# Kernel tuning notes

Measured on AMD Instinct MI355X. Metric: run time of the kernel, lower is better.

The kernel has to match this reference:

```python
import jax, jax.numpy as jnp
import numpy as np

DIM = 768
HEADS = 12
EPS = 1e-5


def setup_inputs() -> dict:
    key = jax.random.key(0)
    ks = jax.random.split(key, 12)
    B, N, C = 2, 2048, DIM
    s = 1.0 / np.sqrt(C)
    return {
        "query": jax.random.normal(ks[0], (B, N, C), jnp.float32),
        "key_in": jax.random.normal(ks[1], (B, N, C), jnp.float32),
        "value": jax.random.normal(ks[2], (B, N, C), jnp.float32),
        "Wq": jax.random.normal(ks[3], (C, C), jnp.float32) * s,
        "bq": jnp.zeros((C,), jnp.float32),
        "Wk": jax.random.normal(ks[4], (C, C), jnp.float32) * s,
        "bk": jnp.zeros((C,), jnp.float32),
        "Wv": jax.random.normal(ks[5], (C, C), jnp.float32) * s,
        "bv": jnp.zeros((C,), jnp.float32),
        "Wo": jax.random.normal(ks[6], (C, C), jnp.float32) * s,
        "bo": jnp.zeros((C,), jnp.float32),
        "gamma": jnp.ones((C,), jnp.float32),
        "beta": jnp.zeros((C,), jnp.float32),
    }


def reference(query, key_in, value, Wq, bq, Wk, bk, Wv, bv, Wo, bo, gamma, beta):
    B, N, C = query.shape
    H = HEADS
    Dh = C // H
    scale = Dh ** (-0.5)
    # projections -> [B, H, N, Dh]
    q = (query @ Wq + bq).reshape(B, N, H, Dh).transpose(0, 2, 1, 3)
    k = (key_in @ Wk + bk).reshape(B, N, H, Dh).transpose(0, 2, 1, 3)
    v = (value @ Wv + bv).reshape(B, N, H, Dh).transpose(0, 2, 1, 3)
    attn = jnp.einsum("bhnd,bhmd->bhnm", q, k) * scale
    attn = jax.nn.softmax(attn, axis=-1)  # dropout is identity in eval mode
    out = jnp.einsum("bhnm,bhmd->bhnd", attn, v)
    out = out.transpose(0, 2, 1, 3).reshape(B, N, C)
    out = out @ Wo + bo
    # residual + LayerNorm
    x = out + query
    mu = jnp.mean(x, axis=-1, keepdims=True)
    var = jnp.mean(jnp.square(x - mu), axis=-1, keepdims=True)
    return (x - mu) * jax.lax.rsqrt(var + EPS) * gamma + beta
```

## Files before the change

kernel.cpp:

```cpp
#include <hip/hip_runtime.h>
#include <hip/hip_bf16.h>


typedef unsigned short ushort_t;
typedef __bf16 bf16x8 __attribute__((ext_vector_type(8)));
typedef float  f32x4  __attribute__((ext_vector_type(4)));
typedef float  f32x16 __attribute__((ext_vector_type(16)));
typedef unsigned int uint32x4 __attribute__((ext_vector_type(4)));
typedef int    i32x2  __attribute__((ext_vector_type(2)));

constexpr int C_DIM  = 768;
constexpr int HEADS  = 12;
constexpr int DH     = 64;
constexpr int BATCH  = 2;
constexpr int SEQ    = 2048;
constexpr int MTOT   = BATCH * SEQ;
constexpr float EPS  = 1e-5f;
constexpr float SCALE = 0.125f;

constexpr size_t SZ_X = (size_t)MTOT * C_DIM;
constexpr size_t SZ_W = (size_t)C_DIM * C_DIM;
constexpr size_t B_XQ  = 0;
constexpr size_t B_XK  = B_XQ  + SZ_X * 2;
constexpr size_t B_XV  = B_XK  + SZ_X * 2;
constexpr size_t B_WQT = B_XV  + SZ_X * 2;
constexpr size_t B_WKT = B_WQT + SZ_W * 2;
constexpr size_t B_WVT = B_WKT + SZ_W * 2;
constexpr size_t B_WOT = B_WVT + SZ_W * 2;
constexpr size_t B_QH  = B_WOT + SZ_W * 2;
constexpr size_t B_KH  = B_QH  + SZ_X * 2;
constexpr size_t B_VT  = B_KH  + SZ_X * 2;
constexpr size_t B_O   = B_VT  + SZ_X * 2;
constexpr size_t B_XR  = B_O   + SZ_X * 2;

__device__ __forceinline__ ushort_t f2bf(float f) {
  __hip_bfloat16 h = __float2bfloat16(f);
  return __builtin_bit_cast(unsigned short, h);
}

__device__ __forceinline__ unsigned cvtpk(float lo, float hi) {
  unsigned r;
  asm("v_cvt_pk_bf16_f32 %0, %1, %2" : "=v"(r) : "v"(lo), "v"(hi));
  return r;
}
__device__ __forceinline__ float xhalf_max(float x) {
  i32x2 r = __builtin_amdgcn_permlane32_swap(
      __builtin_bit_cast(int, x), __builtin_bit_cast(int, x), false, false);
  return fmaxf(__builtin_bit_cast(float, r.x), __builtin_bit_cast(float, r.y));
}
__device__ __forceinline__ float xhalf_sum(float x) {
  i32x2 r = __builtin_amdgcn_permlane32_swap(
      __builtin_bit_cast(int, x), __builtin_bit_cast(int, x), false, false);
  return __builtin_bit_cast(float, r.x) + __builtin_bit_cast(float, r.y);
}

__device__ __forceinline__ void gload_lds16(const void* g, void* l) {
  __builtin_amdgcn_global_load_lds(
      (const __attribute__((address_space(1))) unsigned int*)g,
      (__attribute__((address_space(3))) unsigned int*)l,
      16, 0, 0);
}

__global__ __launch_bounds__(256) void cvt3_kernel(
    const float* __restrict__ s0, const float* __restrict__ s1,
    const float* __restrict__ s2,
    ushort_t* __restrict__ d0, ushort_t* __restrict__ d1,
    ushort_t* __restrict__ d2, int n4) {
  const float* src = blockIdx.y == 0 ? s0 : blockIdx.y == 1 ? s1 : s2;
  ushort_t*    dst = blockIdx.y == 0 ? d0 : blockIdx.y == 1 ? d1 : d2;
  int i = blockIdx.x * 256 + threadIdx.x;
  if (i >= n4) return;
  float4 v = ((const float4*)src)[i];
  ushort4 o;
  o.x = f2bf(v.x); o.y = f2bf(v.y); o.z = f2bf(v.z); o.w = f2bf(v.w);
  ((ushort4*)dst)[i] = o;
}

__global__ __launch_bounds__(256) void wtrans_kernel(
    const float* __restrict__ W0, const float* __restrict__ W1,
    const float* __restrict__ W2, const float* __restrict__ W3,
    ushort_t* T0, ushort_t* T1, ushort_t* T2, ushort_t* T3) {
  const float* W = blockIdx.z == 0 ? W0 : blockIdx.z == 1 ? W1 : blockIdx.z == 2 ? W2 : W3;
  ushort_t*    T = blockIdx.z == 0 ? T0 : blockIdx.z == 1 ? T1 : blockIdx.z == 2 ? T2 : T3;
  __shared__ float tile[32][33];
  int tx = threadIdx.x & 31, ty = threadIdx.x >> 5;
  int x0 = blockIdx.x * 32, y0 = blockIdx.y * 32;
#pragma unroll
  for (int i = 0; i < 32; i += 8)
    tile[ty + i][tx] = W[(size_t)(y0 + ty + i) * C_DIM + x0 + tx];
  __syncthreads();
#pragma unroll
  for (int i = 0; i < 32; i += 8)
    T[(size_t)(x0 + ty + i) * C_DIM + y0 + tx] = f2bf(tile[tx][ty + i]);
}

__device__ __forceinline__ void gemm128_mainloop(
    const ushort_t* __restrict__ A, const ushort_t* __restrict__ Bt,
    int rowBase, int colBase, ushort_t* ldsA, ushort_t* ldsB, f32x4 acc[4][4]) {
  const int tid = threadIdx.x;
  const int wave = tid >> 6, lane = tid & 63;
  const int wr = wave >> 1, wc = wave & 1;
  const int lrow = lane & 15, lk = lane >> 4;
  const int sr = tid >> 2, sk = (tid & 3) * 8;
  const int K = C_DIM;

  const ushort_t* ga0 = A  + (size_t)(rowBase + sr)      * K + sk;
  const ushort_t* ga1 = A  + (size_t)(rowBase + 64 + sr) * K + sk;
  const ushort_t* gb0 = Bt + (size_t)(colBase + sr)      * K + sk;
  const ushort_t* gb1 = Bt + (size_t)(colBase + 64 + sr) * K + sk;
  ushort_t* la = ldsA + sr * 32 + sk;
  ushort_t* lb = ldsB + sr * 32 + sk;

  for (int kt = 0; kt < K; kt += 32) {
    gload_lds16(ga0 + kt, la);
    gload_lds16(ga1 + kt, la + 64 * 32);
    gload_lds16(gb0 + kt, lb);
    gload_lds16(gb1 + kt, lb + 64 * 32);
    asm volatile("s_waitcnt vmcnt(0)" ::: "memory");
    __syncthreads();
    bf16x8 af[4], bfr[4];
#pragma unroll
    for (int m = 0; m < 4; m++)
      af[m] = *(const bf16x8*)(ldsA + (wr * 64 + m * 16 + lrow) * 32 + lk * 8);
#pragma unroll
    for (int n = 0; n < 4; n++)
      bfr[n] = *(const bf16x8*)(ldsB + (wc * 64 + n * 16 + lrow) * 32 + lk * 8);
#pragma unroll
    for (int m = 0; m < 4; m++)
#pragma unroll
      for (int n = 0; n < 4; n++)
        acc[m][n] = __builtin_amdgcn_mfma_f32_16x16x32_bf16(af[m], bfr[n], acc[m][n], 0, 0, 0);
    __syncthreads();
  }
}

__global__ __launch_bounds__(256) void gemm_qkv_kernel(
    const ushort_t* __restrict__ Xq, const ushort_t* __restrict__ Xk,
    const ushort_t* __restrict__ Xv,
    const ushort_t* __restrict__ Wqt, const ushort_t* __restrict__ Wkt,
    const ushort_t* __restrict__ Wvt,
    const float* __restrict__ bq, const float* __restrict__ bk,
    const float* __restrict__ bv,
    ushort_t* Qh, ushort_t* Kh, ushort_t* Vt) {
  const int mat = blockIdx.z;
  const ushort_t* A  = mat == 0 ? Xq  : mat == 1 ? Xk  : Xv;
  const ushort_t* Bt = mat == 0 ? Wqt : mat == 1 ? Wkt : Wvt;
  const float* bias  = mat == 0 ? bq  : mat == 1 ? bk  : bv;

  __shared__ __align__(16) ushort_t ldsA[128 * 32];
  __shared__ __align__(16) ushort_t ldsB[128 * 32];

  const int rowBase = blockIdx.y * 128;
  const int colBase = blockIdx.x * 128;
  f32x4 acc[4][4];
#pragma unroll
  for (int m = 0; m < 4; m++)
#pragma unroll
    for (int n = 0; n < 4; n++)
#pragma unroll
      for (int r = 0; r < 4; r++) acc[m][n][r] = 0.f;

  gemm128_mainloop(A, Bt, rowBase, colBase, ldsA, ldsB, acc);

  const int lane = threadIdx.x & 63, wave = threadIdx.x >> 6;
  const int wr = wave >> 1, wc = wave & 1;
  const int lrow = lane & 15, lk = lane >> 4;
  const float sc = (mat == 0) ? SCALE : 1.0f;

  __hip_bfloat16* dqk = (__hip_bfloat16*)(mat == 0 ? Qh : Kh);
  __hip_bfloat16* dvt = (__hip_bfloat16*)Vt;
#pragma unroll
  for (int n = 0; n < 4; n++) {
    const int col = colBase + wc * 64 + n * 16 + lrow;
    const float bval = bias[col];
    const int hh = col >> 6, dd = col & 63;
#pragma unroll
    for (int m = 0; m < 4; m++) {
#pragma unroll
      for (int r = 0; r < 4; r++) {
        const int row = rowBase + wr * 64 + m * 16 + lk * 4 + r;
        const int bb = row >> 11, nn = row & 2047;
        const float val = (acc[m][n][r] + bval) * sc;
        if (mat < 2) {
          dqk[(((size_t)(bb * HEADS + hh) * SEQ + nn) << 6) + dd] = __float2bfloat16(val);
        } else {
          dvt[((size_t)(bb * HEADS + hh) * DH + dd) * SEQ + nn] = __float2bfloat16(val);
        }
      }
    }
  }
}

__global__ __launch_bounds__(256) void attn_kernel(
    const ushort_t* __restrict__ Qh, const ushort_t* __restrict__ Kh,
    const ushort_t* __restrict__ Vt, ushort_t* __restrict__ O) {
  const int bh = blockIdx.y;
  const int b = bh / HEADS, h = bh % HEADS;
  const ushort_t* Qp = Qh + (size_t)bh * SEQ * DH;
  const ushort_t* Kp = Kh + (size_t)bh * SEQ * DH;
  const ushort_t* Vp = Vt + (size_t)bh * DH * SEQ;

  const int tid = threadIdx.x, wave = tid >> 6, lane = tid & 63;
  const int lq = lane & 31;
  const int hi = lane >> 5;
  const int qrow0 = (blockIdx.x * 4 + wave) * 32;

  bf16x8 qf[4];
#pragma unroll
  for (int ks = 0; ks < 4; ks++)
    qf[ks] = *(const bf16x8*)&Qp[(size_t)(qrow0 + lq) * DH + ks * 16 + hi * 8];

  bf16x8 kfA[4], kfB[4];
#pragma unroll
  for (int ks = 0; ks < 4; ks++)
    kfA[ks] = *(const bf16x8*)&Kp[(size_t)lq * DH + ks * 16 + hi * 8];

  f32x16 oacc[2];
#pragma unroll
  for (int dt = 0; dt < 2; dt++)
#pragma unroll
    for (int r = 0; r < 16; r++) oacc[dt][r] = 0.f;
  float mrun = -3e38f, lrun = 0.f;

#pragma unroll 1
  for (int it = 0; it < SEQ / 32; it++) {
    const int kv = it * 32;
    const bf16x8* kc = (it & 1) ? kfB : kfA;
    bf16x8*       kn = (it & 1) ? kfA : kfB;

    f32x16 st;
#pragma unroll
    for (int r = 0; r < 16; r++) st[r] = 0.f;
#pragma unroll
    for (int ks = 0; ks < 4; ks++)
      st = __builtin_amdgcn_mfma_f32_32x32x16_bf16(kc[ks], qf[ks], st, 0, 0, 0);

    bf16x8 vf[2][2];
#pragma unroll
    for (int dt = 0; dt < 2; dt++)
#pragma unroll
      for (int s = 0; s < 2; s++)
        vf[dt][s] = *(const bf16x8*)&Vp[(size_t)(dt * 32 + lq) * SEQ + kv + s * 16 + hi * 8];

    const int nkv = (kv + 32) & (SEQ - 1);
#pragma unroll
    for (int ks = 0; ks < 4; ks++)
      kn[ks] = *(const bf16x8*)&Kp[(size_t)(nkv + lq) * DH + ks * 16 + hi * 8];

    float tm = st[0];
#pragma unroll
    for (int r = 1; r < 16; r++) tm = fmaxf(tm, st[r]);
    tm = xhalf_max(tm);
    float m = mrun;
    if (!__all(tm <= mrun + 8.f)) {
      m = fmaxf(mrun, tm);
      const float fac = __expf(mrun - m);
      mrun = m;
      lrun *= fac;
#pragma unroll
      for (int dt = 0; dt < 2; dt++)
#pragma unroll
        for (int r = 0; r < 16; r++) oacc[dt][r] *= fac;
    }
    float ps = 0.f;
#pragma unroll
    for (int r = 0; r < 16; r++) {
      float p = __expf(st[r] - m);
      st[r] = p;
      ps += p;
    }
    lrun += xhalf_sum(ps);

    unsigned pk[8];
#pragma unroll
    for (int i = 0; i < 8; i++) pk[i] = cvtpk(st[2 * i], st[2 * i + 1]);
    uint32x4 a0, a1;
    {
      i32x2 r02 = __builtin_amdgcn_permlane32_swap((int)pk[0], (int)pk[2], false, false);
      i32x2 r13 = __builtin_amdgcn_permlane32_swap((int)pk[1], (int)pk[3], false, false);
      a0.x = (unsigned)r02.x; a0.y = (unsigned)r13.x;
      a0.z = (unsigned)r02.y; a0.w = (unsigned)r13.y;
      i32x2 r46 = __builtin_amdgcn_permlane32_swap((int)pk[4], (int)pk[6], false, false);
      i32x2 r57 = __builtin_amdgcn_permlane32_swap((int)pk[5], (int)pk[7], false, false);
      a1.x = (unsigned)r46.x; a1.y = (unsigned)r57.x;
      a1.z = (unsigned)r46.y; a1.w = (unsigned)r57.y;
    }
    const bf16x8 w0 = __builtin_bit_cast(bf16x8, a0);
    const bf16x8 w1 = __builtin_bit_cast(bf16x8, a1);

#pragma unroll
    for (int dt = 0; dt < 2; dt++) {
      oacc[dt] = __builtin_amdgcn_mfma_f32_32x32x16_bf16(vf[dt][0], w0, oacc[dt], 0, 0, 0);
      oacc[dt] = __builtin_amdgcn_mfma_f32_32x32x16_bf16(vf[dt][1], w1, oacc[dt], 0, 0, 0);
    }
  }

  const float inv = 1.f / lrun;
  __hip_bfloat16* Op = (__hip_bfloat16*)O;
  const size_t rowOff = (size_t)(b * SEQ + qrow0 + lq) * C_DIM + h * DH;
#pragma unroll
  for (int dt = 0; dt < 2; dt++)
#pragma unroll
    for (int g = 0; g < 4; g++) {
      ushort4 w;
      w.x = f2bf(oacc[dt][g * 4 + 0] * inv);
      w.y = f2bf(oacc[dt][g * 4 + 1] * inv);
      w.z = f2bf(oacc[dt][g * 4 + 2] * inv);
      w.w = f2bf(oacc[dt][g * 4 + 3] * inv);
      *(ushort4*)&Op[rowOff + dt * 32 + g * 8 + hi * 4] = w;
    }
}

__global__ __launch_bounds__(256) void gemm_out_kernel(
    const ushort_t* __restrict__ Obf, const ushort_t* __restrict__ Wot,
    const float* __restrict__ bo, const float* __restrict__ query,
    float* __restrict__ X) {
  __shared__ __align__(16) ushort_t ldsA[128 * 32];
  __shared__ __align__(16) ushort_t ldsB[128 * 32];
  const int rowBase = blockIdx.y * 128;
  const int colBase = blockIdx.x * 128;
  f32x4 acc[4][4];
#pragma unroll
  for (int m = 0; m < 4; m++)
#pragma unroll
    for (int n = 0; n < 4; n++)
#pragma unroll
      for (int r = 0; r < 4; r++) acc[m][n][r] = 0.f;

  gemm128_mainloop(Obf, Wot, rowBase, colBase, ldsA, ldsB, acc);

  const int lane = threadIdx.x & 63, wave = threadIdx.x >> 6;
  const int wr = wave >> 1, wc = wave & 1;
  const int lrow = lane & 15, lk = lane >> 4;
#pragma unroll
  for (int n = 0; n < 4; n++) {
    const int col = colBase + wc * 64 + n * 16 + lrow;
    const float bval = bo[col];
#pragma unroll
    for (int m = 0; m < 4; m++) {
#pragma unroll
      for (int r = 0; r < 4; r++) {
        const int row = rowBase + wr * 64 + m * 16 + lk * 4 + r;
        const size_t idx = (size_t)row * C_DIM + col;
        X[idx] = acc[m][n][r] + bval + query[idx];
      }
    }
  }
}

__global__ __launch_bounds__(256) void ln_kernel(
    const float* __restrict__ X, const float* __restrict__ gamma,
    const float* __restrict__ beta, float* __restrict__ out) {
  const int row = blockIdx.x, tid = threadIdx.x;
  const float* xr = X + (size_t)row * C_DIM;
  float x0 = xr[tid], x1 = xr[tid + 256], x2 = xr[tid + 512];
  float s = x0 + x1 + x2;
  float sq = x0 * x0 + x1 * x1 + x2 * x2;
#pragma unroll
  for (int off = 32; off; off >>= 1) {
    s  += __shfl_xor(s, off);
    sq += __shfl_xor(sq, off);
  }
  __shared__ float as_[4], aq_[4];
  if ((tid & 63) == 0) { as_[tid >> 6] = s; aq_[tid >> 6] = sq; }
  __syncthreads();
  s  = as_[0] + as_[1] + as_[2] + as_[3];
  sq = aq_[0] + aq_[1] + aq_[2] + aq_[3];
  const float mean = s * (1.f / C_DIM);
  const float var  = sq * (1.f / C_DIM) - mean * mean;
  const float rstd = rsqrtf(var + EPS);
  float* orow = out + (size_t)row * C_DIM;
  orow[tid]       = (x0 - mean) * rstd * gamma[tid]       + beta[tid];
  orow[tid + 256] = (x1 - mean) * rstd * gamma[tid + 256] + beta[tid + 256];
  orow[tid + 512] = (x2 - mean) * rstd * gamma[tid + 512] + beta[tid + 512];
}

extern "C" void kernel_launch(void* const* d_in, const int* in_sizes, int n_in,
                              void* d_out, int out_size, void* d_ws, size_t ws_size,
                              hipStream_t stream) {
  (void)in_sizes; (void)n_in; (void)out_size; (void)ws_size;
  const float* query  = (const float*)d_in[0];
  const float* key_in = (const float*)d_in[1];
  const float* value  = (const float*)d_in[2];
  const float* Wq = (const float*)d_in[3];
  const float* bq = (const float*)d_in[4];
  const float* Wk = (const float*)d_in[5];
  const float* bk = (const float*)d_in[6];
  const float* Wv = (const float*)d_in[7];
  const float* bv = (const float*)d_in[8];
  const float* Wo = (const float*)d_in[9];
  const float* bo = (const float*)d_in[10];
  const float* gamma = (const float*)d_in[11];
  const float* beta  = (const float*)d_in[12];

  char* ws = (char*)d_ws;
  ushort_t* Xq  = (ushort_t*)(ws + B_XQ);
  ushort_t* Xk  = (ushort_t*)(ws + B_XK);
  ushort_t* Xv  = (ushort_t*)(ws + B_XV);
  ushort_t* Wqt = (ushort_t*)(ws + B_WQT);
  ushort_t* Wkt = (ushort_t*)(ws + B_WKT);
  ushort_t* Wvt = (ushort_t*)(ws + B_WVT);
  ushort_t* Wot = (ushort_t*)(ws + B_WOT);
  ushort_t* Qh  = (ushort_t*)(ws + B_QH);
  ushort_t* Kh  = (ushort_t*)(ws + B_KH);
  ushort_t* Vt  = (ushort_t*)(ws + B_VT);
  ushort_t* Obf = (ushort_t*)(ws + B_O);
  float*    Xr  = (float*)(ws + B_XR);
  float*    out = (float*)d_out;

  const int n4 = (int)(SZ_X / 4);
  cvt3_kernel<<<dim3(n4 / 256, 3), 256, 0, stream>>>(query, key_in, value,
                                                     Xq, Xk, Xv, n4);

  wtrans_kernel<<<dim3(24, 24, 4), 256, 0, stream>>>(Wq, Wk, Wv, Wo, Wqt, Wkt, Wvt, Wot);

  gemm_qkv_kernel<<<dim3(6, 32, 3), 256, 0, stream>>>(Xq, Xk, Xv, Wqt, Wkt, Wvt,
                                                      bq, bk, bv, Qh, Kh, Vt);

  attn_kernel<<<dim3(SEQ / 128, BATCH * HEADS), 256, 0, stream>>>(Qh, Kh, Vt, Obf);

  gemm_out_kernel<<<dim3(6, 32), 256, 0, stream>>>(Obf, Wot, bo, query, Xr);

  ln_kernel<<<MTOT, 256, 0, stream>>>(Xr, gamma, beta, out);
}
```

Measured before the change: 290.7 us.

## Split attention KV range in two, XCD-aware block mapping, and add combine kernel

Attention now splits each head's KV sequence into two halves processed by separate blocks, doubling the grid from 384 to 768 blocks. Each block writes unnormalized bf16 partial outputs plus running max and sum to workspace, and a new combine kernel merges the halves and writes the final layout. Block indices are remapped so each head stays on one XCD, and s_setprio brackets the MFMA sections. The cost is an extra launch, extra partial-output memory traffic, and bf16 rounding of the unnormalized partials.

New measurement: 277.7 us. 1.05x faster.

```diff
diff --git a/kernel.cpp b/kernel.cpp
--- a/kernel.cpp
+++ b/kernel.cpp
@@ -15,6 +15,9 @@
 constexpr int BATCH  = 2;
 constexpr int SEQ    = 2048;
 constexpr int MTOT   = BATCH * SEQ;
+constexpr int MROWS  = BATCH * HEADS * SEQ;
+constexpr int NSPLIT = 2;
+constexpr int KVSPAN = SEQ / NSPLIT;
 constexpr float EPS  = 1e-5f;
 constexpr float SCALE = 0.125f;
 
@@ -32,6 +35,8 @@
 constexpr size_t B_VT  = B_KH  + SZ_X * 2;
 constexpr size_t B_O   = B_VT  + SZ_X * 2;
 constexpr size_t B_XR  = B_O   + SZ_X * 2;
+constexpr size_t B_OP  = B_XQ;
+constexpr size_t B_ML  = B_OP + (size_t)NSPLIT * MROWS * DH * 2;
 
 __device__ __forceinline__ ushort_t f2bf(float f) {
   __hip_bfloat16 h = __float2bfloat16(f);
@@ -193,9 +198,17 @@
 
 __global__ __launch_bounds__(256) void attn_kernel(
     const ushort_t* __restrict__ Qh, const ushort_t* __restrict__ Kh,
-    const ushort_t* __restrict__ Vt, ushort_t* __restrict__ O) {
-  const int bh = blockIdx.y;
-  const int b = bh / HEADS, h = bh % HEADS;
+    const ushort_t* __restrict__ Vt, ushort_t* __restrict__ Opart,
+    float2* __restrict__ Ml) {
+  const int fb   = blockIdx.x;
+  const int xcd  = fb & 7;
+  const int slot = fb >> 3;
+  const int g    = slot >> 5;
+  const int rem  = slot & 31;
+  const int qt    = rem & 15;
+  const int split = rem >> 4;
+  const int bh    = xcd + 8 * g;
+
   const ushort_t* Qp = Qh + (size_t)bh * SEQ * DH;
   const ushort_t* Kp = Kh + (size_t)bh * SEQ * DH;
   const ushort_t* Vp = Vt + (size_t)bh * DH * SEQ;
@@ -203,7 +216,8 @@
   const int tid = threadIdx.x, wave = tid >> 6, lane = tid & 63;
   const int lq = lane & 31;
   const int hi = lane >> 5;
-  const int qrow0 = (blockIdx.x * 4 + wave) * 32;
+  const int qrow0 = qt * 128 + wave * 32;
+  const int kv0 = split * KVSPAN;
 
   bf16x8 qf[4];
 #pragma unroll
@@ -213,7 +227,7 @@
   bf16x8 kfA[4], kfB[4];
 #pragma unroll
   for (int ks = 0; ks < 4; ks++)
-    kfA[ks] = *(const bf16x8*)&Kp[(size_t)lq * DH + ks * 16 + hi * 8];
+    kfA[ks] = *(const bf16x8*)&Kp[(size_t)(kv0 + lq) * DH + ks * 16 + hi * 8];
 
   f32x16 oacc[2];
 #pragma unroll
@@ -223,17 +237,19 @@
   float mrun = -3e38f, lrun = 0.f;
 
 #pragma unroll 1
-  for (int it = 0; it < SEQ / 32; it++) {
-    const int kv = it * 32;
+  for (int it = 0; it < KVSPAN / 32; it++) {
+    const int kv = kv0 + it * 32;
     const bf16x8* kc = (it & 1) ? kfB : kfA;
     bf16x8*       kn = (it & 1) ? kfA : kfB;
 
     f32x16 st;
 #pragma unroll
     for (int r = 0; r < 16; r++) st[r] = 0.f;
+    __builtin_amdgcn_s_setprio(1);
 #pragma unroll
     for (int ks = 0; ks < 4; ks++)
       st = __builtin_amdgcn_mfma_f32_32x32x16_bf16(kc[ks], qf[ks], st, 0, 0, 0);
+    __builtin_amdgcn_s_setprio(0);
 
     bf16x8 vf[2][2];
 #pragma unroll
@@ -242,7 +258,7 @@
       for (int s = 0; s < 2; s++)
         vf[dt][s] = *(const bf16x8*)&Vp[(size_t)(dt * 32 + lq) * SEQ + kv + s * 16 + hi * 8];
 
-    const int nkv = (kv + 32) & (SEQ - 1);
+    const int nkv = kv0 + (((it + 1) & (KVSPAN / 32 - 1)) * 32);
 #pragma unroll
     for (int ks = 0; ks < 4; ks++)
       kn[ks] = *(const bf16x8*)&Kp[(size_t)(nkv + lq) * DH + ks * 16 + hi * 8];
@@ -288,27 +304,51 @@
     const bf16x8 w0 = __builtin_bit_cast(bf16x8, a0);
     const bf16x8 w1 = __builtin_bit_cast(bf16x8, a1);
 
+    __builtin_amdgcn_s_setprio(1);
 #pragma unroll
     for (int dt = 0; dt < 2; dt++) {
       oacc[dt] = __builtin_amdgcn_mfma_f32_32x32x16_bf16(vf[dt][0], w0, oacc[dt], 0, 0, 0);
       oacc[dt] = __builtin_amdgcn_mfma_f32_32x32x16_bf16(vf[dt][1], w1, oacc[dt], 0, 0, 0);
     }
+    __builtin_amdgcn_s_setprio(0);
   }
 
-  const float inv = 1.f / lrun;
-  __hip_bfloat16* Op = (__hip_bfloat16*)O;
-  const size_t rowOff = (size_t)(b * SEQ + qrow0 + lq) * C_DIM + h * DH;
+  const int rid = bh * SEQ + qrow0 + lq;
+  ushort_t* Oprow = Opart + ((size_t)split * MROWS + rid) * DH;
 #pragma unroll
   for (int dt = 0; dt < 2; dt++)
 #pragma unroll
-    for (int g = 0; g < 4; g++) {
+    for (int gg = 0; gg < 4; gg++) {
       ushort4 w;
-      w.x = f2bf(oacc[dt][g * 4 + 0] * inv);
-      w.y = f2bf(oacc[dt][g * 4 + 1] * inv);
-      w.z = f2bf(oacc[dt][g * 4 + 2] * inv);
-      w.w = f2bf(oacc[dt][g * 4 + 3] * inv);
-      *(ushort4*)&Op[rowOff + dt * 32 + g * 8 + hi * 4] = w;
-    }
+      w.x = f2bf(oacc[dt][gg * 4 + 0]);
+      w.y = f2bf(oacc[dt][gg * 4 + 1]);
+      w.z = f2bf(oacc[dt][gg * 4 + 2]);
+      w.w = f2bf(oacc[dt][gg * 4 + 3]);
+      *(ushort4*)&Oprow[dt * 32 + gg * 8 + hi * 4] = w;
+    }
+  if (hi == 0) Ml[(size_t)split * MROWS + rid] = make_float2(mrun, lrun);
+}
+
+__global__ __launch_bounds__(256) void attn_combine_kernel(
+    const ushort_t* __restrict__ Opart, const float2* __restrict__ Ml,
+    ushort_t* __restrict__ O) {
+  const int t = threadIdx.x;
+  const int rid = blockIdx.x * 4 + (t >> 6);
+  const int col = t & 63;
+  const float2 ml0 = Ml[rid];
+  const float2 ml1 = Ml[(size_t)MROWS + rid];
+  const float M = fmaxf(ml0.x, ml1.x);
+  const float w0 = __expf(ml0.x - M), w1 = __expf(ml1.x - M);
+  const float inv = 1.f / (w0 * ml0.y + w1 * ml1.y);
+  const float o0 = __bfloat162float(__builtin_bit_cast(__hip_bfloat16,
+                     Opart[(size_t)rid * DH + col]));
+  const float o1 = __bfloat162float(__builtin_bit_cast(__hip_bfloat16,
+                     Opart[((size_t)MROWS + rid) * DH + col]));
+  const float o = (w0 * o0 + w1 * o1) * inv;
+  const int bh = rid >> 11, n = rid & 2047;
+  const int b = bh / HEADS, h = bh - b * HEADS;
+  ((__hip_bfloat16*)O)[(size_t)(b * SEQ + n) * C_DIM + h * DH + col] =
+      __float2bfloat16(o);
 }
 
 __global__ __launch_bounds__(256) void gemm_out_kernel(
@@ -406,6 +446,8 @@
   ushort_t* Vt  = (ushort_t*)(ws + B_VT);
   ushort_t* Obf = (ushort_t*)(ws + B_O);
   float*    Xr  = (float*)(ws + B_XR);
+  ushort_t* Opart = (ushort_t*)(ws + B_OP);
+  float2*   Ml    = (float2*)(ws + B_ML);
   float*    out = (float*)d_out;
 
   const int n4 = (int)(SZ_X / 4);
@@ -417,7 +459,9 @@
   gemm_qkv_kernel<<<dim3(6, 32, 3), 256, 0, stream>>>(Xq, Xk, Xv, Wqt, Wkt, Wvt,
                                                       bq, bk, bv, Qh, Kh, Vt);
 
-  attn_kernel<<<dim3(SEQ / 128, BATCH * HEADS), 256, 0, stream>>>(Qh, Kh, Vt, Obf);
+  attn_kernel<<<8 * 3 * 16 * NSPLIT, 256, 0, stream>>>(Qh, Kh, Vt, Opart, Ml);
+
+  attn_combine_kernel<<<MROWS / 4, 256, 0, stream>>>(Opart, Ml, Obf);
 
   gemm_out_kernel<<<dim3(6, 32), 256, 0, stream>>>(Obf, Wot, bo, query, Xr);
 
```
